# Performance work log

Hardware: AMD Instinct MI355X
Metric: run time of the kernel (lower is better)

## Reference

```python
import jax, jax.numpy as jnp
import numpy as np

N_NODES = 50000
N_EDGES = 800000
NUM_FEAT = 256
HID = 64
N_CLS = 40
N_LAYERS = 2
EPS = 0.3  # residual scale from __init__ eps


def setup_inputs() -> dict:
    key = jax.random.key(0)
    ks = jax.random.split(key, 8)
    x = jax.random.normal(ks[0], (N_NODES, NUM_FEAT), dtype=jnp.float32)
    edge_index = jax.random.randint(ks[1], (2, N_EDGES), 0, N_NODES, dtype=jnp.int64)
    # xavier-normal-ish scaled weights
    W1 = jax.random.normal(ks[2], (HID, NUM_FEAT), dtype=jnp.float32) * (1.414 * (2.0 / (HID + NUM_FEAT)) ** 0.5)
    b1 = jnp.zeros((HID,), dtype=jnp.float32)
    W2 = jax.random.normal(ks[3], (N_CLS, HID), dtype=jnp.float32) * (1.414 * (2.0 / (N_CLS + HID)) ** 0.5)
    b2 = jnp.zeros((N_CLS,), dtype=jnp.float32)
    gate_w = jax.random.normal(ks[4], (N_LAYERS, 2 * HID), dtype=jnp.float32) * (1.414 * (2.0 / (2 * HID + 1)) ** 0.5)
    gate_b = jnp.zeros((N_LAYERS,), dtype=jnp.float32)
    return {"x": x, "edge_index": edge_index, "W1": W1, "b1": b1,
            "W2": W2, "b2": b2, "gate_w": gate_w, "gate_b": gate_b}


def _forward(x, edge_index, W1, b1, W2, b2, gate_w, gate_b):
    row, col = edge_index[0], edge_index[1]  # row = source, col = target (PyG convention)
    n = x.shape[0]
    ones_e = jnp.ones((edge_index.shape[1],), dtype=x.dtype)
    # degree(row) clamped to >=1, then d^{-1/2}
    deg = jnp.clip(jax.ops.segment_sum(ones_e, row, num_segments=n), 1.0)
    nd = deg ** -0.5  # [N]
    # mean-aggregation denominator: incoming-edge counts per target node
    cnt = jnp.clip(jax.ops.segment_sum(ones_e, col, num_segments=n), 1.0)

    # dense input projection (dropout is eval-mode no-op)
    h = jax.nn.relu(x @ W1.T + b1)  # [N, H]
    raw = h

    nd_edge = nd[row] * nd[col]  # [E]
    for l in range(N_LAYERS):
        hr = h[row]  # [E, H] gather (source)
        hc = h[col]  # [E, H] gather (target)
        # gate: Linear(concat([h[row], h[col]])) == h[row]@w_a + h[col]@w_b
        g = jnp.tanh(hr @ gate_w[l, :HID] + hc @ gate_w[l, HID:] + gate_b[l])  # [E]
        norm = g * nd_edge  # [E]
        msg = norm[:, None] * (hc + hr)  # x_i + x_j, [E, H]
        agg = jax.ops.segment_sum(msg, col, num_segments=n) / cnt[:, None]  # scatter-mean
        h = EPS * raw + agg

    logits = h @ W2.T + b2
    return jax.nn.log_softmax(logits, axis=1)


def reference(x, edge_index, W1, b1, W2, b2, gate_w, gate_b):
    return _forward(x, edge_index, W1, b1, W2, b2, gate_w, gate_b)
```

## Files before the change

### kernel.cpp

```cpp
#include <hip/hip_runtime.h>
#include <math.h>

#define N_NODES 50000
#define N_EDGES 800000
#define NFEAT 256
#define HID 64
#define NCLS 40
#define EPS_RES 0.3f
#define ROWSZ 68
#define SCAN_BLOCKS ((N_NODES + 255) / 256)
#define EB 32
#define CHUNK (N_EDGES / EB)
#define NR 4
#define RNG (N_NODES / NR)

typedef unsigned int uint;
typedef unsigned short ushort;

__device__ __forceinline__ float bflo(uint u) { return __uint_as_float(u << 16); }
__device__ __forceinline__ float bfhi(uint u) { return __uint_as_float(u & 0xFFFF0000u); }
__device__ __forceinline__ uint bf16rne(float f) {
    uint u = __float_as_uint(f);
    return (u + 0x7FFFu + ((u >> 16) & 1u)) >> 16;
}
__device__ __forceinline__ uint bf16rne2(float a, float b) {
    return bf16rne(a) | (bf16rne(b) << 16);
}

__device__ __forceinline__ float fast_tanh(float x) {
    float t = __builtin_amdgcn_exp2f(x * 2.885390081777927f);
    return 1.0f - 2.0f * __builtin_amdgcn_rcpf(t + 1.0f);
}

__global__ __launch_bounds__(256) void hist_kernel(const int* __restrict__ row,
                                                   const int* __restrict__ col,
                                                   int* __restrict__ degM,
                                                   int* __restrict__ cntM,
                                                   int* __restrict__ rank_local) {
    __shared__ int hist[RNG];
    int t = threadIdx.x;
    int chunk = blockIdx.x;
    int lo = blockIdx.y * RNG;
    int side = blockIdx.z;
    for (int j = t; j < RNG; j += 256) hist[j] = 0;
    __syncthreads();
    const int* idx = side ? col : row;
    int e0 = chunk * CHUNK;
    if (side == 0) {
        for (int base = 0; base < CHUNK; base += 1024) {
            int vb[4];
#pragma unroll
            for (int j = 0; j < 4; j++) {
                int i = base + j * 256 + t;
                vb[j] = (i < CHUNK) ? idx[e0 + i] : -1;
            }
#pragma unroll
            for (int j = 0; j < 4; j++) {
                uint v = (uint)(vb[j] - lo);
                if (v < RNG) atomicAdd(&hist[v], 1);
            }
        }
    } else {
        for (int base = 0; base < CHUNK; base += 1024) {
            int vb[4], ib[4];
#pragma unroll
            for (int j = 0; j < 4; j++) {
                int i = base + j * 256 + t;
                ib[j] = i;
                vb[j] = (i < CHUNK) ? idx[e0 + i] : -1;
            }
#pragma unroll
            for (int j = 0; j < 4; j++) {
                uint v = (uint)(vb[j] - lo);
                if (v < RNG) rank_local[e0 + ib[j]] = atomicAdd(&hist[v], 1);
            }
        }
    }
    __syncthreads();
    int* M = side ? cntM : degM;
    for (int j = t; j < RNG; j += 256) M[chunk * N_NODES + lo + j] = hist[j];
}

__device__ __forceinline__ int block_excl_scan_256(int v, int t, int* wsum) {
    int lane = t & 63, w = t >> 6;
    int sv = v;
#pragma unroll
    for (int d = 1; d < 64; d <<= 1) {
        int o = __shfl_up(sv, d);
        if (lane >= d) sv += o;
    }
    if (lane == 63) wsum[w] = sv;
    __syncthreads();
    int add = 0;
    for (int i = 0; i < w; i++) add += wsum[i];
    return sv + add - v;
}

__global__ void scan1_kernel(const int* __restrict__ degM, int* __restrict__ cntM,
                             int* __restrict__ off, int* __restrict__ bsum,
                             float* __restrict__ nd, float* __restrict__ invcnt) {
    __shared__ int wsum[4];
    int t = threadIdx.x;
    int idx = blockIdx.x * 256 + t;
    int v = 0;
    if (idx < N_NODES) {
        int sD = 0;
#pragma unroll
        for (int c = 0; c < EB; c++) sD += degM[c * N_NODES + idx];
        int run = 0;
#pragma unroll
        for (int c = 0; c < EB; c++) {
            int cv = cntM[c * N_NODES + idx];
            cntM[c * N_NODES + idx] = run;
            run += cv;
        }
        v = run;
        if (sD < 1) sD = 1;
        nd[idx] = rsqrtf((float)sD);
        int cc = run; if (cc < 1) cc = 1;
        invcnt[idx] = 1.0f / (float)cc;
    }
    int excl = block_excl_scan_256(v, t, wsum);
    if (idx < N_NODES) off[idx] = excl;
    if (t == 255) bsum[blockIdx.x] = excl + v;
}

__global__ void scan2_kernel(int* __restrict__ bsum) {
    __shared__ int wsum[4];
    int t = threadIdx.x;
    int v = (t < SCAN_BLOCKS) ? bsum[t] : 0;
    int excl = block_excl_scan_256(v, t, wsum);
    if (t < SCAN_BLOCKS) bsum[t] = excl;
}

__global__ void scan3_kernel(int* __restrict__ off, const int* __restrict__ bsum) {
    int t = threadIdx.x;
    int idx = blockIdx.x * 256 + t;
    if (idx < N_NODES) off[idx] += bsum[blockIdx.x];
    if (idx == 0) off[N_NODES] = N_EDGES;
}

__global__ void scatter_kernel(const int* __restrict__ row, const int* __restrict__ col,
                               const int* __restrict__ rank_local, const int* __restrict__ cntM,
                               const int* __restrict__ off, const float* __restrict__ nd,
                               int2* __restrict__ sedge) {
    int e = blockIdx.x * 256 + threadIdx.x;
    int r = row[e], c = col[e];
    int ch = e / CHUNK;
    int p = off[c] + cntM[ch * N_NODES + c] + rank_local[e];
    int2 se;
    se.x = r;
    se.y = __float_as_int(nd[r] * nd[c]);
    sedge[p] = se;
}

__global__ __launch_bounds__(256) void proj_kernel(const float* __restrict__ x,
                                                   const float* __restrict__ W1,
                                                   const float* __restrict__ b1,
                                                   const float* __restrict__ gw,
                                                   float* __restrict__ ha,
                                                   ushort* __restrict__ habf,
                                                   float* __restrict__ y,
                                                   float* __restrict__ z) {
    __shared__ float xs[64 * ROWSZ];
    __shared__ float ws[64 * ROWSZ];
    int t = threadIdx.x;
    int nb = blockIdx.x * 64;
    int lane = t & 63, w = t >> 6;
    int l15 = lane & 15, g = lane >> 4;
    int hbase = 16 * w + 4 * g;
    float acc[4][4];
#pragma unroll
    for (int j = 0; j < 4; j++)
#pragma unroll
        for (int i = 0; i < 4; i++) acc[j][i] = 0.f;

    for (int kc = 0; kc < NFEAT; kc += 64) {
        __syncthreads();
#pragma unroll
        for (int i = 0; i < 4; i++) {
            int idx = t + 256 * i;
            int r_ = idx >> 4;
            int kq = idx & 15;
            int gn = nb + r_;
            float4 v = make_float4(0.f, 0.f, 0.f, 0.f);
            if (gn < N_NODES) v = *(const float4*)(x + (size_t)gn * NFEAT + kc + kq * 4);
            *(float4*)(xs + r_ * ROWSZ + kq * 4) = v;
            float4 wv = *(const float4*)(W1 + (size_t)r_ * NFEAT + kc + kq * 4);
            *(float4*)(ws + r_ * ROWSZ + kq * 4) = wv;
        }
        __syncthreads();
#pragma unroll 4
        for (int k = 0; k < 64; k += 4) {
            float4 a[4], b[4];
#pragma unroll
            for (int j = 0; j < 4; j++) a[j] = *(const float4*)(xs + (l15 + 16 * j) * ROWSZ + k);
#pragma unroll
            for (int i = 0; i < 4; i++) b[i] = *(const float4*)(ws + (hbase + i) * ROWSZ + k);
#pragma unroll
            for (int j = 0; j < 4; j++)
#pragma unroll
                for (int i = 0; i < 4; i++)
                    acc[j][i] += a[j].x * b[i].x + a[j].y * b[i].y + a[j].z * b[i].z + a[j].w * b[i].w;
        }
    }
    float4 bias = *(const float4*)(b1 + hbase);
    float4 wa4 = *(const float4*)(gw + hbase);
    float4 wb4 = *(const float4*)(gw + HID + hbase);
    int slot = w * 4 + g;
    __syncthreads();
#pragma unroll
    for (int j = 0; j < 4; j++) {
        int gn = nb + l15 + 16 * j;
        float4 o;
        o.x = fmaxf(acc[j][0] + bias.x, 0.f);
        o.y = fmaxf(acc[j][1] + bias.y, 0.f);
        o.z = fmaxf(acc[j][2] + bias.z, 0.f);
        o.w = fmaxf(acc[j][3] + bias.w, 0.f);
        if (gn < N_NODES) {
            *(float4*)(ha + (size_t)gn * HID + hbase) = o;
            uint2 pk;
            pk.x = bf16rne2(o.x, o.y);
            pk.y = bf16rne2(o.z, o.w);
            *(uint2*)(habf + (size_t)gn * HID + hbase) = pk;
        }
        xs[(l15 + 16 * j) * 16 + slot] = o.x * wa4.x + o.y * wa4.y + o.z * wa4.z + o.w * wa4.w;
        ws[(l15 + 16 * j) * 16 + slot] = o.x * wb4.x + o.y * wb4.y + o.z * wb4.z + o.w * wb4.w;
    }
    __syncthreads();
    if (t < 64 && nb + t < N_NODES) {
        float sa = 0.f, sb = 0.f;
#pragma unroll
        for (int s = 0; s < 16; s++) { sa += xs[t * 16 + s]; sb += ws[t * 16 + s]; }
        y[nb + t] = sa;
        z[nb + t] = sb;
    }
}

__device__ __forceinline__ void agg_group8(const ushort* __restrict__ hbf,
                                           const int2* __restrict__ sedge,
                                           const float* __restrict__ yv,
                                           float zc, int e0, int d, int c8,
                                           float acc[8], float& gs_out) {
#pragma unroll
    for (int i = 0; i < 8; i++) acc[i] = 0.f;
    float gs = 0.f;
    int m = d;
    m = max(m, __shfl_xor(m, 8));
    m = max(m, __shfl_xor(m, 16));
    m = max(m, __shfl_xor(m, 32));
    if (m > 0) {
        int2 seA = sedge[(0 < d) ? e0 : 0];
        float ndeA = (0 < d) ? __int_as_float(seA.y) : 0.f;
        int2 seB = sedge[(1 < d) ? e0 + 1 : 0];
        float ndeB = (1 < d) ? __int_as_float(seB.y) : 0.f;
        int2 seC = sedge[(2 < d) ? e0 + 2 : 0];
        float ndeC = (2 < d) ? __int_as_float(seC.y) : 0.f;
        float yA = yv[seA.x];
        uint4 uA = *(const uint4*)(hbf + (size_t)seA.x * HID + c8);
        float yB = yv[seB.x];
        uint4 uB = *(const uint4*)(hbf + (size_t)seB.x * HID + c8);
        for (int k = 0; k < m; ++k) {
            float yC = yv[seC.x];
            uint4 uC = *(const uint4*)(hbf + (size_t)seC.x * HID + c8);
            int kD = k + 3;
            int2 seD = sedge[(kD < d) ? e0 + kD : 0];
            float ndeD = (kD < d) ? __int_as_float(seD.y) : 0.f;
            float gv = fast_tanh(yA + zc) * ndeA;
            acc[0] += gv * bflo(uA.x);
            acc[1] += gv * bfhi(uA.x);
            acc[2] += gv * bflo(uA.y);
            acc[3] += gv * bfhi(uA.y);
            acc[4] += gv * bflo(uA.z);
            acc[5] += gv * bfhi(uA.z);
            acc[6] += gv * bflo(uA.w);
            acc[7] += gv * bfhi(uA.w);
            gs += gv;
            yA = yB; uA = uB; ndeA = ndeB;
            yB = yC; uB = uC; ndeB = ndeC;
            seC = seD; ndeC = ndeD;
        }
    }
    gs_out = gs;
}

__global__ __launch_bounds__(256) void agg1_kernel(
        const float* __restrict__ ha, const ushort* __restrict__ habf,
        const int2* __restrict__ sedge, const int* __restrict__ off,
        const float* __restrict__ invcnt, const float* __restrict__ y,
        const float* __restrict__ z, const float* __restrict__ gb,
        const float* __restrict__ gw2, ushort* __restrict__ hbbf,
        float* __restrict__ y2, float* __restrict__ z2) {
    int t = threadIdx.x;
    int lane = t & 63;
    int ln = t >> 3;
    int node = blockIdx.x * 32 + ln;
    int nc = (node < N_NODES) ? node : (N_NODES - 1);
    int c8 = (lane & 7) * 8;
    int e0 = off[nc];
    int e1 = off[nc + 1];
    int d = (node < N_NODES) ? (e1 - e0) : 0;
    float zc = z[nc] + gb[0];
    float acc[8]; float gs;
    agg_group8(habf, sedge, y, zc, e0, d, c8, acc, gs);
    float invc = invcnt[nc];
    float4 ra = *(const float4*)(ha + (size_t)nc * HID + c8);
    float4 rb = *(const float4*)(ha + (size_t)nc * HID + c8 + 4);
    float raw8[8] = {ra.x, ra.y, ra.z, ra.w, rb.x, rb.y, rb.z, rb.w};
    float o[8];
#pragma unroll
    for (int i = 0; i < 8; i++) o[i] = EPS_RES * raw8[i] + (acc[i] + gs * raw8[i]) * invc;
    if (node < N_NODES) {
        uint4 pk;
        pk.x = bf16rne2(o[0], o[1]);
        pk.y = bf16rne2(o[2], o[3]);
        pk.z = bf16rne2(o[4], o[5]);
        pk.w = bf16rne2(o[6], o[7]);
        *(uint4*)(hbbf + (size_t)nc * HID + c8) = pk;
    }
    float4 wa0 = *(const float4*)(gw2 + c8);
    float4 wa1 = *(const float4*)(gw2 + c8 + 4);
    float4 wb0 = *(const float4*)(gw2 + HID + c8);
    float4 wb1 = *(const float4*)(gw2 + HID + c8 + 4);
    float p = o[0] * wa0.x + o[1] * wa0.y + o[2] * wa0.z + o[3] * wa0.w
            + o[4] * wa1.x + o[5] * wa1.y + o[6] * wa1.z + o[7] * wa1.w;
    float qq = o[0] * wb0.x + o[1] * wb0.y + o[2] * wb0.z + o[3] * wb0.w
             + o[4] * wb1.x + o[5] * wb1.y + o[6] * wb1.z + o[7] * wb1.w;
#pragma unroll
    for (int s = 1; s < 8; s <<= 1) { p += __shfl_xor(p, s); qq += __shfl_xor(qq, s); }
    if ((lane & 7) == 0 && node < N_NODES) { y2[node] = p; z2[node] = qq; }
}

__global__ __launch_bounds__(256) void agg2_kernel(
        const ushort* __restrict__ hbbf, const float* __restrict__ ha,
        const int2* __restrict__ sedge, const int* __restrict__ off,
        const float* __restrict__ invcnt, const float* __restrict__ y2,
        const float* __restrict__ z2, const float* __restrict__ gb,
        const float* __restrict__ W2, const float* __restrict__ b2,
        float* __restrict__ out) {
    __shared__ float w2s[NCLS * 72];
    __shared__ float b2s[NCLS];
    __shared__ float hs[32 * 72];
    int t = threadIdx.x;
    for (int i = t; i < NCLS * HID; i += 256) w2s[(i >> 6) * 72 + (i & 63)] = W2[i];
    if (t < NCLS) b2s[t] = b2[t];
    int lane = t & 63;
    int ln = t >> 3;
    int node = blockIdx.x * 32 + ln;
    int nc = (node < N_NODES) ? node : (N_NODES - 1);
    int c8 = (lane & 7) * 8;
    int e0 = off[nc];
    int e1 = off[nc + 1];
    int d = (node < N_NODES) ? (e1 - e0) : 0;
    float zc = z2[nc] + gb[0];
    float acc[8]; float gs;
    agg_group8(hbbf, sedge, y2, zc, e0, d, c8, acc, gs);
    float invc = invcnt[nc];
    uint4 hc = *(const uint4*)(hbbf + (size_t)nc * HID + c8);
    float hcv[8] = {bflo(hc.x), bfhi(hc.x), bflo(hc.y), bfhi(hc.y),
                    bflo(hc.z), bfhi(hc.z), bflo(hc.w), bfhi(hc.w)};
    float4 ra = *(const float4*)(ha + (size_t)nc * HID + c8);
    float4 rb = *(const float4*)(ha + (size_t)nc * HID + c8 + 4);
    float raw8[8] = {ra.x, ra.y, ra.z, ra.w, rb.x, rb.y, rb.z, rb.w};
    float4 o0, o1;
    o0.x = EPS_RES * raw8[0] + (acc[0] + gs * hcv[0]) * invc;
    o0.y = EPS_RES * raw8[1] + (acc[1] + gs * hcv[1]) * invc;
    o0.z = EPS_RES * raw8[2] + (acc[2] + gs * hcv[2]) * invc;
    o0.w = EPS_RES * raw8[3] + (acc[3] + gs * hcv[3]) * invc;
    o1.x = EPS_RES * raw8[4] + (acc[4] + gs * hcv[4]) * invc;
    o1.y = EPS_RES * raw8[5] + (acc[5] + gs * hcv[5]) * invc;
    o1.z = EPS_RES * raw8[6] + (acc[6] + gs * hcv[6]) * invc;
    o1.w = EPS_RES * raw8[7] + (acc[7] + gs * hcv[7]) * invc;
    *(float4*)(hs + ln * 72 + c8) = o0;
    *(float4*)(hs + ln * 72 + c8 + 4) = o1;
    __syncthreads();
    int k5 = t & 7;
    float lg[5];
#pragma unroll
    for (int j = 0; j < 5; j++) lg[j] = b2s[k5 + 8 * j];
    const float* hrow = hs + ln * 72;
#pragma unroll
    for (int j4 = 0; j4 < 16; j4++) {
        float4 h4 = *(const float4*)(hrow + j4 * 4);
#pragma unroll
        for (int j = 0; j < 5; j++) {
            float4 w4 = *(const float4*)(w2s + (k5 + 8 * j) * 72 + j4 * 4);
            lg[j] += h4.x * w4.x + h4.y * w4.y + h4.z * w4.z + h4.w * w4.w;
        }
    }
    float v = fmaxf(fmaxf(fmaxf(lg[0], lg[1]), fmaxf(lg[2], lg[3])), lg[4]);
    v = fmaxf(v, __shfl_xor(v, 1));
    v = fmaxf(v, __shfl_xor(v, 2));
    v = fmaxf(v, __shfl_xor(v, 4));
    float ex = 0.f;
#pragma unroll
    for (int j = 0; j < 5; j++) ex += __builtin_amdgcn_exp2f((lg[j] - v) * 1.44269504088896f);
    ex += __shfl_xor(ex, 1);
    ex += __shfl_xor(ex, 2);
    ex += __shfl_xor(ex, 4);
    float ls = v + __builtin_amdgcn_logf(ex) * 0.693147180559945f;
    if (node < N_NODES) {
#pragma unroll
        for (int j = 0; j < 5; j++) out[(size_t)node * NCLS + k5 + 8 * j] = lg[j] - ls;
    }
}

extern "C" void kernel_launch(void* const* d_in, const int* in_sizes, int n_in,
                              void* d_out, int out_size, void* d_ws, size_t ws_size,
                              hipStream_t stream) {
    const float* x  = (const float*)d_in[0];
    const int*   ei = (const int*)d_in[1];
    const float* W1 = (const float*)d_in[2];
    const float* b1 = (const float*)d_in[3];
    const float* W2 = (const float*)d_in[4];
    const float* b2 = (const float*)d_in[5];
    const float* gw = (const float*)d_in[6];
    const float* gb = (const float*)d_in[7];
    float* out = (float*)d_out;

    int2*  sedge  = (int2*)d_ws;
    float* nd     = (float*)(sedge + N_EDGES);
    float* invcnt = nd + N_NODES;
    float* y      = invcnt + N_NODES;
    float* z      = y + N_NODES;
    float* y2     = z + N_NODES;
    float* z2     = y2 + N_NODES;
    float* ha     = z2 + N_NODES;
    ushort* habf  = (ushort*)(ha + (size_t)N_NODES * HID);
    ushort* hbbf  = habf + (size_t)N_NODES * HID;
    int*   off    = (int*)(hbbf + (size_t)N_NODES * HID);
    int*   bsum   = off + N_NODES + 1;
    int*   degM   = (int*)ha;
    int*   cntM   = degM + (size_t)EB * N_NODES;
    int*   rank_local = (int*)habf;

    const int* row = ei;
    const int* col = ei + N_EDGES;

    hist_kernel<<<dim3(EB, NR, 2), 256, 0, stream>>>(row, col, degM, cntM, rank_local);
    scan1_kernel<<<SCAN_BLOCKS, 256, 0, stream>>>(degM, cntM, off, bsum, nd, invcnt);
    scan2_kernel<<<1, 256, 0, stream>>>(bsum);
    scan3_kernel<<<SCAN_BLOCKS, 256, 0, stream>>>(off, bsum);
    scatter_kernel<<<N_EDGES / 256, 256, 0, stream>>>(row, col, rank_local, cntM, off, nd, sedge);
    proj_kernel<<<(N_NODES + 63) / 64, 256, 0, stream>>>(x, W1, b1, gw, ha, habf, y, z);

    int aggblocks = (N_NODES + 31) / 32;
    agg1_kernel<<<aggblocks, 256, 0, stream>>>(ha, habf, sedge, off, invcnt, y, z, gb,
                                               gw + 2 * HID, hbbf, y2, z2);
    agg2_kernel<<<aggblocks, 256, 0, stream>>>(hbbf, ha, sedge, off, invcnt, y2, z2,
                                               gb + 1, W2, b2, out);
}
```

Before: 235.3 us.

## Use split-bf16 MFMA for input projection GEMM instead of FP32 FMA

The dense x@W1^T projection moves from scalar FP32 dot products in shared memory to MFMA 16x16x32 bf16 instructions. Each FP32 operand is split into high and low bf16 halves, and three MFMA products (hh, hl, lh) approximate FP32 accuracy. Accumulators are staged through shared memory to restore the original per-thread output layout for the bias, ReLU, bf16 pack and gate-dot epilogue. This targets the compute cost of the projection but adds conversion work, an extra LDS round trip and a small precision loss from dropping the low-low term.

Result: faster. 220.9 us (-6.1%).

```diff
diff --git a/kernel.cpp b/kernel.cpp
--- a/kernel.cpp
+++ b/kernel.cpp
@@ -7,7 +7,6 @@
 #define HID 64
 #define NCLS 40
 #define EPS_RES 0.3f
-#define ROWSZ 68
 #define SCAN_BLOCKS ((N_NODES + 255) / 256)
 #define EB 32
 #define CHUNK (N_EDGES / EB)
@@ -16,6 +15,8 @@
 
 typedef unsigned int uint;
 typedef unsigned short ushort;
+typedef __attribute__((ext_vector_type(8))) short short8v;
+typedef __attribute__((ext_vector_type(4))) float f32x4;
 
 __device__ __forceinline__ float bflo(uint u) { return __uint_as_float(u << 16); }
 __device__ __forceinline__ float bfhi(uint u) { return __uint_as_float(u & 0xFFFF0000u); }
@@ -25,6 +26,14 @@
 }
 __device__ __forceinline__ uint bf16rne2(float a, float b) {
     return bf16rne(a) | (bf16rne(b) << 16);
+}
+
+__device__ __forceinline__ void bfsplit(float v, ushort& h, ushort& l) {
+    uint hb_ = bf16rne(v);
+    float hf = __uint_as_float(hb_ << 16);
+    uint lb_ = bf16rne(v - hf);
+    h = (ushort)hb_;
+    l = (ushort)lb_;
 }
 
 __device__ __forceinline__ float fast_tanh(float x) {
@@ -162,18 +171,20 @@
                                                    ushort* __restrict__ habf,
                                                    float* __restrict__ y,
                                                    float* __restrict__ z) {
-    __shared__ float xs[64 * ROWSZ];
-    __shared__ float ws[64 * ROWSZ];
+    __shared__ ushort smem[4 * 64 * 72];
+    ushort* xs_h = smem;
+    ushort* xs_l = smem + 4608;
+    ushort* ws_h = smem + 9216;
+    ushort* ws_l = smem + 13824;
     int t = threadIdx.x;
     int nb = blockIdx.x * 64;
     int lane = t & 63, w = t >> 6;
     int l15 = lane & 15, g = lane >> 4;
     int hbase = 16 * w + 4 * g;
-    float acc[4][4];
-#pragma unroll
-    for (int j = 0; j < 4; j++)
-#pragma unroll
-        for (int i = 0; i < 4; i++) acc[j][i] = 0.f;
+
+    f32x4 acc[4];
+#pragma unroll
+    for (int hb = 0; hb < 4; hb++) acc[hb] = (f32x4)0.f;
 
     for (int kc = 0; kc < NFEAT; kc += 64) {
         __syncthreads();
@@ -185,38 +196,67 @@
             int gn = nb + r_;
             float4 v = make_float4(0.f, 0.f, 0.f, 0.f);
             if (gn < N_NODES) v = *(const float4*)(x + (size_t)gn * NFEAT + kc + kq * 4);
-            *(float4*)(xs + r_ * ROWSZ + kq * 4) = v;
+            ushort4 h4, l4;
+            bfsplit(v.x, h4.x, l4.x);
+            bfsplit(v.y, h4.y, l4.y);
+            bfsplit(v.z, h4.z, l4.z);
+            bfsplit(v.w, h4.w, l4.w);
+            *(ushort4*)(xs_h + r_ * 72 + kq * 4) = h4;
+            *(ushort4*)(xs_l + r_ * 72 + kq * 4) = l4;
             float4 wv = *(const float4*)(W1 + (size_t)r_ * NFEAT + kc + kq * 4);
-            *(float4*)(ws + r_ * ROWSZ + kq * 4) = wv;
+            bfsplit(wv.x, h4.x, l4.x);
+            bfsplit(wv.y, h4.y, l4.y);
+            bfsplit(wv.z, h4.z, l4.z);
+            bfsplit(wv.w, h4.w, l4.w);
+            *(ushort4*)(ws_h + r_ * 72 + kq * 4) = h4;
+            *(ushort4*)(ws_l + r_ * 72 + kq * 4) = l4;
         }
         __syncthreads();
-#pragma unroll 4
-        for (int k = 0; k < 64; k += 4) {
-            float4 a[4], b[4];
-#pragma unroll
-            for (int j = 0; j < 4; j++) a[j] = *(const float4*)(xs + (l15 + 16 * j) * ROWSZ + k);
-#pragma unroll
-            for (int i = 0; i < 4; i++) b[i] = *(const float4*)(ws + (hbase + i) * ROWSZ + k);
-#pragma unroll
-            for (int j = 0; j < 4; j++)
-#pragma unroll
-                for (int i = 0; i < 4; i++)
-                    acc[j][i] += a[j].x * b[i].x + a[j].y * b[i].y + a[j].z * b[i].z + a[j].w * b[i].w;
-        }
-    }
+#pragma unroll
+        for (int ko = 0; ko < 2; ko++) {
+            int koff = ko * 32 + g * 8;
+            short8v a_h = *(const short8v*)(xs_h + (w * 16 + l15) * 72 + koff);
+            short8v a_l = *(const short8v*)(xs_l + (w * 16 + l15) * 72 + koff);
+            short8v b_h[4], b_l[4];
+#pragma unroll
+            for (int hb = 0; hb < 4; hb++) {
+                b_h[hb] = *(const short8v*)(ws_h + (hb * 16 + l15) * 72 + koff);
+                b_l[hb] = *(const short8v*)(ws_l + (hb * 16 + l15) * 72 + koff);
+            }
+#pragma unroll
+            for (int hb = 0; hb < 4; hb++) {
+                acc[hb] = __builtin_amdgcn_mfma_f32_16x16x32_bf16(a_h, b_h[hb], acc[hb], 0, 0, 0);
+                acc[hb] = __builtin_amdgcn_mfma_f32_16x16x32_bf16(a_h, b_l[hb], acc[hb], 0, 0, 0);
+                acc[hb] = __builtin_amdgcn_mfma_f32_16x16x32_bf16(a_l, b_h[hb], acc[hb], 0, 0, 0);
+            }
+        }
+    }
+    __syncthreads();
+    float* hsf = (float*)smem;
+    float* ypart = hsf + 64 * 68;
+    float* zpart = ypart + 1024;
+#pragma unroll
+    for (int hb = 0; hb < 4; hb++)
+#pragma unroll
+        for (int r = 0; r < 4; r++) {
+            int nl = w * 16 + g * 4 + r;
+            hsf[nl * 68 + hb * 16 + l15] = acc[hb][r];
+        }
+    __syncthreads();
     float4 bias = *(const float4*)(b1 + hbase);
     float4 wa4 = *(const float4*)(gw + hbase);
     float4 wb4 = *(const float4*)(gw + HID + hbase);
     int slot = w * 4 + g;
-    __syncthreads();
 #pragma unroll
     for (int j = 0; j < 4; j++) {
-        int gn = nb + l15 + 16 * j;
+        int rowl = l15 + 16 * j;
+        int gn = nb + rowl;
+        float4 hv = *(const float4*)(hsf + rowl * 68 + hbase);
         float4 o;
-        o.x = fmaxf(acc[j][0] + bias.x, 0.f);
-        o.y = fmaxf(acc[j][1] + bias.y, 0.f);
-        o.z = fmaxf(acc[j][2] + bias.z, 0.f);
-        o.w = fmaxf(acc[j][3] + bias.w, 0.f);
+        o.x = fmaxf(hv.x + bias.x, 0.f);
+        o.y = fmaxf(hv.y + bias.y, 0.f);
+        o.z = fmaxf(hv.z + bias.z, 0.f);
+        o.w = fmaxf(hv.w + bias.w, 0.f);
         if (gn < N_NODES) {
             *(float4*)(ha + (size_t)gn * HID + hbase) = o;
             uint2 pk;
@@ -224,14 +264,14 @@
             pk.y = bf16rne2(o.z, o.w);
             *(uint2*)(habf + (size_t)gn * HID + hbase) = pk;
         }
-        xs[(l15 + 16 * j) * 16 + slot] = o.x * wa4.x + o.y * wa4.y + o.z * wa4.z + o.w * wa4.w;
-        ws[(l15 + 16 * j) * 16 + slot] = o.x * wb4.x + o.y * wb4.y + o.z * wb4.z + o.w * wb4.w;
+        ypart[rowl * 16 + slot] = o.x * wa4.x + o.y * wa4.y + o.z * wa4.z + o.w * wa4.w;
+        zpart[rowl * 16 + slot] = o.x * wb4.x + o.y * wb4.y + o.z * wb4.z + o.w * wb4.w;
     }
     __syncthreads();
     if (t < 64 && nb + t < N_NODES) {
         float sa = 0.f, sb = 0.f;
 #pragma unroll
-        for (int s = 0; s < 16; s++) { sa += xs[t * 16 + s]; sb += ws[t * 16 + s]; }
+        for (int s = 0; s < 16; s++) { sa += ypart[t * 16 + s]; sb += zpart[t * 16 + s]; }
         y[nb + t] = sa;
         z[nb + t] = sb;
     }
```
